# Performance work log

Hardware: AMD Instinct MI355X
Metric: run time of the kernel (lower is better)

The kernel has to match this reference:

```python
import jax, jax.numpy as jnp
import numpy as np

KSIZE = 15
SIGMA = 3.0
PAD = KSIZE // 2


def _gauss_kernel2d():
    g = jnp.arange(KSIZE, dtype=jnp.float32) - KSIZE // 2
    g = jnp.exp(-(g ** 2) / (2.0 * SIGMA * SIGMA))
    g = g / g.sum()
    return g[:, None] * g[None, :]  # [15,15]


def _depthwise_blur(x, k2):
    # x: [B,C,H,W]; 15x15 Gaussian applied per channel (matches per-channel F.conv2d loop)
    C = x.shape[1]
    kernel = jnp.broadcast_to(k2[None, None], (C, 1, KSIZE, KSIZE))
    return jax.lax.conv_general_dilated(
        x, kernel, window_strides=(1, 1), padding=[(PAD, PAD), (PAD, PAD)],
        feature_group_count=C, dimension_numbers=("NCHW", "OIHW", "NCHW"))


def setup_inputs() -> dict:
    key = jax.random.key(0)
    B, C, H, W = 4, 3, 1024, 1024
    x = jax.random.uniform(key, (B, C, H, W), dtype=jnp.float32)
    f32 = lambda v: jnp.asarray(v, dtype=jnp.float32)
    return {
        "x": x,
        "gains": jnp.array([1.1, 1.0, 0.9], dtype=jnp.float32),
        "gamma": f32(0.9),
        "shadow_boost": f32(0.1),
        "highlight_reduce": f32(0.1),
        "brightness": f32(0.05),
        "contrast": f32(1.1),
        "enhance_amount": f32(0.8),
        "softness": f32(0.6),
        "intensity": f32(0.3),
        "rotation": f32(30.0),
        "hardness": f32(2.0),
    }


def reference(x, gains, gamma, shadow_boost, highlight_reduce, brightness,
              contrast, enhance_amount, softness, intensity, rotation, hardness):
    B, C, H, W = x.shape
    k2 = _gauss_kernel2d()

    # WhiteBalanceAdjustment
    x = x * gains.reshape(1, C, 1, 1)
    # ToneCurveAdjustment
    x = jnp.power(x, gamma)
    # ShadowHighlightEnhancement
    hi = jax.nn.sigmoid((x - 0.5) * 10.0)
    x = jnp.clip(x + shadow_boost * (1.0 - hi) - highlight_reduce * hi, 0.0, 1.0)
    # GlobalBrightnessContrastAdjustment
    x = jnp.clip(contrast * (x - 0.5) + 0.5 + brightness, 0.0, 1.0)
    # LocalContrastEnhancement
    local_mean = _depthwise_blur(x, k2)
    x = x + enhance_amount * (x - local_mean)
    # SoftnessFilter
    blurred = _depthwise_blur(x, k2)
    x = softness * blurred + (1.0 - softness) * x
    # GradientNDAdjustment
    ys = jnp.linspace(-1.0, 1.0, H, dtype=jnp.float32)
    xs = jnp.linspace(-1.0, 1.0, W, dtype=jnp.float32)
    grid_y, grid_x = jnp.meshgrid(ys, xs, indexing="ij")
    theta = rotation * (np.pi / 180.0)
    grid_rot = grid_x * jnp.cos(theta) + grid_y * jnp.sin(theta)
    mask = jax.nn.sigmoid(-hardness * grid_rot)[None, None]  # [1,1,H,W]
    x = jnp.clip(x * (1.0 - intensity * mask), 0.0, 1.0)

    return jnp.clip(x, 0.0, 1.0)
```

## Files before the change

### kernel.cpp

```cpp
#include <hip/hip_runtime.h>
#include <math.h>

#define HH 1024
#define WW 1024
#define NPLANES 12
#define PLANE (HH * WW)
#define NTOT (NPLANES * PLANE)

#define TW 64
#define TH 64
#define HR 78
#define PADW 68

struct W15 { float w[15]; };

__global__ __launch_bounds__(256) void k_point(
    const float4* __restrict__ x, float4* __restrict__ o,
    const float* __restrict__ gains,
    const float* __restrict__ pg, const float* __restrict__ psb,
    const float* __restrict__ phr, const float* __restrict__ pbr,
    const float* __restrict__ pct)
{
    int i = blockIdx.x * blockDim.x + threadIdx.x;
    if (i >= NTOT / 4) return;
    int c = ((i * 4) / PLANE) % 3;
    float gain = gains[c];
    float gamma = *pg, sb = *psb, hr = *phr, br = *pbr, ct = *pct;

    float4 v = x[i];
    float* pv = (float*)&v;
#pragma unroll
    for (int j = 0; j < 4; ++j) {
        float t = pv[j] * gain;
        t = __builtin_amdgcn_exp2f(gamma * __log2f(t));
        float hi = __fdividef(1.0f, 1.0f + __expf((0.5f - t) * 10.0f));
        t = t + sb * (1.0f - hi) - hr * hi;
        t = fminf(fmaxf(t, 0.0f), 1.0f);
        t = ct * (t - 0.5f) + 0.5f + br;
        t = fminf(fmaxf(t, 0.0f), 1.0f);
        pv[j] = t;
    }
    o[i] = v;
}

__device__ inline float4 ld4z(const float* __restrict__ row, int x) {
    if (x >= 0 && x + 3 < WW) return *(const float4*)(row + x);
    float4 r; float* p = (float*)&r;
#pragma unroll
    for (int j = 0; j < 4; ++j) { int xx = x + j; p[j] = (xx >= 0 && xx < WW) ? row[xx] : 0.0f; }
    return r;
}

template<int MODE>
__global__ __launch_bounds__(256) void k_blur_fused(
    const float* __restrict__ src, float* __restrict__ dst,
    const float* __restrict__ s0, const float* __restrict__ s1,
    const float* __restrict__ s2, const float* __restrict__ s3, W15 wk)
{
    __shared__ float hbl[HR * PADW];
    const int p   = blockIdx.z;
    const int x0  = blockIdx.x * TW;
    const int y0  = blockIdx.y * TH;
    const int tid = threadIdx.x;
    const float* plane = src + (size_t)p * PLANE;

    {
        const int cx = (tid & 15) * 4;
        const int r0 = tid >> 4;
#pragma unroll
        for (int it = 0; it < 5; ++it) {
            int r = r0 + 16 * it;
            if (r < HR) {
                int y = y0 - 7 + r;
                float4 o;
                if (y >= 0 && y < HH) {
                    const float* row = plane + (size_t)y * WW;
                    int xb = x0 + cx - 8;
                    float f[20];
                    *(float4*)&f[0]  = ld4z(row, xb);
                    *(float4*)&f[4]  = ld4z(row, xb + 4);
                    *(float4*)&f[8]  = ld4z(row, xb + 8);
                    *(float4*)&f[12] = ld4z(row, xb + 12);
                    *(float4*)&f[16] = ld4z(row, xb + 16);
                    float* po = (float*)&o;
#pragma unroll
                    for (int j = 0; j < 4; ++j) {
                        float acc = 0.0f;
#pragma unroll
                        for (int k = 0; k < 15; ++k) acc += wk.w[k] * f[j + 1 + k];
                        po[j] = acc;
                    }
                } else {
                    o = make_float4(0.0f, 0.0f, 0.0f, 0.0f);
                }
                *(float4*)&hbl[r * PADW + cx] = o;
            }
        }
    }
    __syncthreads();

    const int tx  = tid & 63;
    const int ty  = tid >> 6;
    const int ly0 = ty * 16;
    const int x   = x0 + tx;

    float win[15];
#pragma unroll
    for (int k = 0; k < 15; ++k) win[k] = hbl[(ly0 + k) * PADW + tx];

    float a0 = *s0;
    float a1 = 0.f, sth = 0.f, hard = 0.f, base = 0.f;
    if (MODE == 1) {
        a1 = *s1;
        float theta = (*s2) * 0.017453292519943295f;
        float cth = __cosf(theta); sth = __sinf(theta);
        hard = *s3;
        float gx = -1.0f + 2.0f * (float)x * (1.0f / (float)(WW - 1));
        base = gx * cth;
    }

    float* dstP = dst + (size_t)p * PLANE;

#pragma unroll
    for (int j = 0; j < 16; ++j) {
        int y = y0 + ly0 + j;
        float bl = 0.0f;
#pragma unroll
        for (int k = 0; k < 15; ++k) bl += wk.w[k] * win[k];
        float c = plane[(size_t)y * WW + x];
        float v;
        if (MODE == 0) {
            v = (1.0f + a0) * c - a0 * bl;
        } else {
            v = a0 * bl + (1.0f - a0) * c;
            float gy = -1.0f + 2.0f * (float)y * (1.0f / (float)(HH - 1));
            float gr = base + gy * sth;
            float mask = __fdividef(1.0f, 1.0f + __expf(hard * gr));
            v = v * (1.0f - a1 * mask);
            v = fminf(fmaxf(v, 0.0f), 1.0f);
        }
        dstP[(size_t)y * WW + x] = v;
#pragma unroll
        for (int k = 0; k < 14; ++k) win[k] = win[k + 1];
        win[14] = hbl[(ly0 + j + 15) * PADW + tx];
    }
}

extern "C" void kernel_launch(void* const* d_in, const int* in_sizes, int n_in,
                              void* d_out, int out_size, void* d_ws, size_t ws_size,
                              hipStream_t stream)
{
    const float* x       = (const float*)d_in[0];
    const float* gains   = (const float*)d_in[1];
    const float* p_gamma = (const float*)d_in[2];
    const float* p_sb    = (const float*)d_in[3];
    const float* p_hr    = (const float*)d_in[4];
    const float* p_br    = (const float*)d_in[5];
    const float* p_ct    = (const float*)d_in[6];
    const float* p_enh   = (const float*)d_in[7];
    const float* p_soft  = (const float*)d_in[8];
    const float* p_int   = (const float*)d_in[9];
    const float* p_rot   = (const float*)d_in[10];
    const float* p_hard  = (const float*)d_in[11];

    float* A = (float*)d_out;
    float* B = (float*)d_ws;

    W15 wk;
    {
        double g[15], sum = 0.0;
        for (int i = 0; i < 15; ++i) { double d = (double)(i - 7); g[i] = exp(-d * d / 18.0); sum += g[i]; }
        for (int i = 0; i < 15; ++i) wk.w[i] = (float)(g[i] / sum);
    }

    k_point<<<dim3(NTOT / 4 / 256), dim3(256), 0, stream>>>(
        (const float4*)x, (float4*)A, gains, p_gamma, p_sb, p_hr, p_br, p_ct);

    dim3 g(WW / TW, HH / TH, NPLANES);
    k_blur_fused<0><<<g, dim3(256), 0, stream>>>(A, B, p_enh, p_enh, p_enh, p_enh, wk);
    k_blur_fused<1><<<g, dim3(256), 0, stream>>>(B, A, p_soft, p_int, p_rot, p_hard, wk);
}
```

Baseline: 200.3 us.

## Fuse pointwise tone chain into first blur kernel and enlarge final blur tile

The separate pointwise kernel is removed. Each first-blur block now loads its haloed tile of raw input, applies the white-balance/tone/contrast chain while staging it into shared memory, and then blurs from there, which saves one full read and write of the intermediate image. The cost is recomputing the transcendental chain on halo pixels, about 1.6x the pixel count, plus more shared memory per block. The final blur kernel also switches to 128-row tiles with 32 rows per thread, which cuts the vertical halo overhead but halves the block count and raises register pressure.

```diff
diff --git a/kernel.cpp b/kernel.cpp
--- a/kernel.cpp
+++ b/kernel.cpp
@@ -9,73 +9,147 @@
 
 #define TW 64
 #define TH 64
-#define HR 78
-#define PADW 68
+#define HRA 78
+#define RAWP 84
+#define HBLP 68
+
+#define TH2 128
+#define HRB 142
 
 struct W15 { float w[15]; };
 
-__global__ __launch_bounds__(256) void k_point(
-    const float4* __restrict__ x, float4* __restrict__ o,
+__device__ inline float4 ld4z(const float* __restrict__ row, int x) {
+    if (x >= 0 && x + 3 < WW) return *(const float4*)(row + x);
+    float4 r; float* p = (float*)&r;
+#pragma unroll
+    for (int j = 0; j < 4; ++j) { int xx = x + j; p[j] = (xx >= 0 && xx < WW) ? row[xx] : 0.0f; }
+    return r;
+}
+
+__device__ inline float chain1(float t, float gain, float gamma, float sb,
+                               float hr, float br, float ct) {
+    t = t * gain;
+    t = __builtin_amdgcn_exp2f(gamma * __log2f(t));
+    float hi = __fdividef(1.0f, 1.0f + __expf((0.5f - t) * 10.0f));
+    t = t + sb * (1.0f - hi) - hr * hi;
+    t = fminf(fmaxf(t, 0.0f), 1.0f);
+    t = ct * (t - 0.5f) + 0.5f + br;
+    return fminf(fmaxf(t, 0.0f), 1.0f);
+}
+
+__global__ __launch_bounds__(256) void k_chain_blur_lce(
+    const float* __restrict__ x, float* __restrict__ dst,
     const float* __restrict__ gains,
     const float* __restrict__ pg, const float* __restrict__ psb,
     const float* __restrict__ phr, const float* __restrict__ pbr,
-    const float* __restrict__ pct)
+    const float* __restrict__ pct, const float* __restrict__ penh, W15 wk)
 {
-    int i = blockIdx.x * blockDim.x + threadIdx.x;
-    if (i >= NTOT / 4) return;
-    int c = ((i * 4) / PLANE) % 3;
-    float gain = gains[c];
-    float gamma = *pg, sb = *psb, hr = *phr, br = *pbr, ct = *pct;
-
-    float4 v = x[i];
-    float* pv = (float*)&v;
-#pragma unroll
-    for (int j = 0; j < 4; ++j) {
-        float t = pv[j] * gain;
-        t = __builtin_amdgcn_exp2f(gamma * __log2f(t));
-        float hi = __fdividef(1.0f, 1.0f + __expf((0.5f - t) * 10.0f));
-        t = t + sb * (1.0f - hi) - hr * hi;
-        t = fminf(fmaxf(t, 0.0f), 1.0f);
-        t = ct * (t - 0.5f) + 0.5f + br;
-        t = fminf(fmaxf(t, 0.0f), 1.0f);
-        pv[j] = t;
-    }
-    o[i] = v;
-}
-
-__device__ inline float4 ld4z(const float* __restrict__ row, int x) {
-    if (x >= 0 && x + 3 < WW) return *(const float4*)(row + x);
-    float4 r; float* p = (float*)&r;
-#pragma unroll
-    for (int j = 0; j < 4; ++j) { int xx = x + j; p[j] = (xx >= 0 && xx < WW) ? row[xx] : 0.0f; }
-    return r;
-}
-
-template<int MODE>
-__global__ __launch_bounds__(256) void k_blur_fused(
-    const float* __restrict__ src, float* __restrict__ dst,
-    const float* __restrict__ s0, const float* __restrict__ s1,
-    const float* __restrict__ s2, const float* __restrict__ s3, W15 wk)
-{
-    __shared__ float hbl[HR * PADW];
+    __shared__ float raw[HRA * RAWP];
+    __shared__ float hbl[HRA * HBLP];
     const int p   = blockIdx.z;
     const int x0  = blockIdx.x * TW;
     const int y0  = blockIdx.y * TH;
     const int tid = threadIdx.x;
-    const float* plane = src + (size_t)p * PLANE;
+    const float* plane = x + (size_t)p * PLANE;
+
+    const float gain  = gains[p % 3];
+    const float gamma = *pg, sb = *psb, hr = *phr, br = *pbr, ct = *pct;
+    const float e     = *penh;
+
+    for (int i = tid; i < HRA * 20; i += 256) {
+        int r  = i / 20;
+        int c4 = i % 20;
+        int y  = y0 - 7 + r;
+        int xb = x0 - 8 + c4 * 4;
+        float4 v;
+        if (y >= 0 && y < HH) {
+            float4 f = ld4z(plane + (size_t)y * WW, xb);
+            float* pf = (float*)&f; float* pv = (float*)&v;
+#pragma unroll
+            for (int j = 0; j < 4; ++j) {
+                float cv = chain1(pf[j], gain, gamma, sb, hr, br, ct);
+                int xx = xb + j;
+                pv[j] = (xx >= 0 && xx < WW) ? cv : 0.0f;
+            }
+        } else {
+            v = make_float4(0.0f, 0.0f, 0.0f, 0.0f);
+        }
+        *(float4*)&raw[r * RAWP + c4 * 4] = v;
+    }
+    __syncthreads();
 
     {
-        const int cx = (tid & 15) * 4;
+        const int c4 = (tid & 15) * 4;
         const int r0 = tid >> 4;
 #pragma unroll
         for (int it = 0; it < 5; ++it) {
             int r = r0 + 16 * it;
-            if (r < HR) {
+            if (r < HRA) {
+                float f[20];
+#pragma unroll
+                for (int m = 0; m < 5; ++m)
+                    *(float4*)&f[4 * m] = *(const float4*)&raw[r * RAWP + c4 + 4 * m];
+                float4 o; float* po = (float*)&o;
+#pragma unroll
+                for (int j = 0; j < 4; ++j) {
+                    float acc = 0.0f;
+#pragma unroll
+                    for (int k = 0; k < 15; ++k) acc += wk.w[k] * f[j + 1 + k];
+                    po[j] = acc;
+                }
+                *(float4*)&hbl[r * HBLP + c4] = o;
+            }
+        }
+    }
+    __syncthreads();
+
+    const int tx  = tid & 63;
+    const int ty  = tid >> 6;
+    const int ly0 = ty * 16;
+
+    float win[15];
+#pragma unroll
+    for (int k = 0; k < 15; ++k) win[k] = hbl[(ly0 + k) * HBLP + tx];
+
+    float* dstP = dst + (size_t)p * PLANE;
+#pragma unroll
+    for (int j = 0; j < 16; ++j) {
+        int y = y0 + ly0 + j;
+        float lm = 0.0f;
+#pragma unroll
+        for (int k = 0; k < 15; ++k) lm += wk.w[k] * win[k];
+        float c = raw[(ly0 + j + 7) * RAWP + tx + 8];
+        dstP[(size_t)y * WW + x0 + tx] = (1.0f + e) * c - e * lm;
+#pragma unroll
+        for (int k = 0; k < 14; ++k) win[k] = win[k + 1];
+        win[14] = hbl[(ly0 + j + 15) * HBLP + tx];
+    }
+}
+
+__global__ __launch_bounds__(256) void k_blur_final(
+    const float* __restrict__ src, float* __restrict__ dst,
+    const float* __restrict__ psoft, const float* __restrict__ pint,
+    const float* __restrict__ prot, const float* __restrict__ phard, W15 wk)
+{
+    __shared__ float hbl[HRB * HBLP];
+    const int p   = blockIdx.z;
+    const int x0  = blockIdx.x * TW;
+    const int y0  = blockIdx.y * TH2;
+    const int tid = threadIdx.x;
+    const float* plane = src + (size_t)p * PLANE;
+
+    {
+        const int c4 = (tid & 15) * 4;
+        const int r0 = tid >> 4;
+#pragma unroll
+        for (int it = 0; it < 9; ++it) {
+            int r = r0 + 16 * it;
+            if (r < HRB) {
                 int y = y0 - 7 + r;
                 float4 o;
                 if (y >= 0 && y < HH) {
                     const float* row = plane + (size_t)y * WW;
-                    int xb = x0 + cx - 8;
+                    int xb = x0 + c4 - 8;
                     float f[20];
                     *(float4*)&f[0]  = ld4z(row, xb);
                     *(float4*)&f[4]  = ld4z(row, xb + 4);
@@ -93,7 +167,7 @@
                 } else {
                     o = make_float4(0.0f, 0.0f, 0.0f, 0.0f);
                 }
-                *(float4*)&hbl[r * PADW + cx] = o;
+                *(float4*)&hbl[r * HBLP + c4] = o;
             }
         }
     }
@@ -101,48 +175,37 @@
 
     const int tx  = tid & 63;
     const int ty  = tid >> 6;
-    const int ly0 = ty * 16;
+    const int ly0 = ty * 32;
     const int x   = x0 + tx;
 
+    const float s     = *psoft;
+    const float inten = *pint;
+    const float hard  = *phard;
+    const float theta = (*prot) * 0.017453292519943295f;
+    const float cth = __cosf(theta), sth = __sinf(theta);
+    const float base = (-1.0f + 2.0f * (float)x * (1.0f / (float)(WW - 1))) * cth;
+
     float win[15];
 #pragma unroll
-    for (int k = 0; k < 15; ++k) win[k] = hbl[(ly0 + k) * PADW + tx];
-
-    float a0 = *s0;
-    float a1 = 0.f, sth = 0.f, hard = 0.f, base = 0.f;
-    if (MODE == 1) {
-        a1 = *s1;
-        float theta = (*s2) * 0.017453292519943295f;
-        float cth = __cosf(theta); sth = __sinf(theta);
-        hard = *s3;
-        float gx = -1.0f + 2.0f * (float)x * (1.0f / (float)(WW - 1));
-        base = gx * cth;
-    }
+    for (int k = 0; k < 15; ++k) win[k] = hbl[(ly0 + k) * HBLP + tx];
 
     float* dstP = dst + (size_t)p * PLANE;
-
-#pragma unroll
-    for (int j = 0; j < 16; ++j) {
+#pragma unroll
+    for (int j = 0; j < 32; ++j) {
         int y = y0 + ly0 + j;
         float bl = 0.0f;
 #pragma unroll
         for (int k = 0; k < 15; ++k) bl += wk.w[k] * win[k];
         float c = plane[(size_t)y * WW + x];
-        float v;
-        if (MODE == 0) {
-            v = (1.0f + a0) * c - a0 * bl;
-        } else {
-            v = a0 * bl + (1.0f - a0) * c;
-            float gy = -1.0f + 2.0f * (float)y * (1.0f / (float)(HH - 1));
-            float gr = base + gy * sth;
-            float mask = __fdividef(1.0f, 1.0f + __expf(hard * gr));
-            v = v * (1.0f - a1 * mask);
-            v = fminf(fmaxf(v, 0.0f), 1.0f);
-        }
+        float v = s * bl + (1.0f - s) * c;
+        float gy = -1.0f + 2.0f * (float)y * (1.0f / (float)(HH - 1));
+        float mask = __fdividef(1.0f, 1.0f + __expf(hard * (base + gy * sth)));
+        v = v * (1.0f - inten * mask);
+        v = fminf(fmaxf(v, 0.0f), 1.0f);
         dstP[(size_t)y * WW + x] = v;
 #pragma unroll
         for (int k = 0; k < 14; ++k) win[k] = win[k + 1];
-        win[14] = hbl[(ly0 + j + 15) * PADW + tx];
+        win[14] = hbl[(ly0 + j + 15) * HBLP + tx];
     }
 }
 
@@ -163,8 +226,8 @@
     const float* p_rot   = (const float*)d_in[10];
     const float* p_hard  = (const float*)d_in[11];
 
-    float* A = (float*)d_out;
-    float* B = (float*)d_ws;
+    float* X2  = (float*)d_ws;
+    float* OUT = (float*)d_out;
 
     W15 wk;
     {
@@ -173,10 +236,11 @@
         for (int i = 0; i < 15; ++i) wk.w[i] = (float)(g[i] / sum);
     }
 
-    k_point<<<dim3(NTOT / 4 / 256), dim3(256), 0, stream>>>(
-        (const float4*)x, (float4*)A, gains, p_gamma, p_sb, p_hr, p_br, p_ct);
-
-    dim3 g(WW / TW, HH / TH, NPLANES);
-    k_blur_fused<0><<<g, dim3(256), 0, stream>>>(A, B, p_enh, p_enh, p_enh, p_enh, wk);
-    k_blur_fused<1><<<g, dim3(256), 0, stream>>>(B, A, p_soft, p_int, p_rot, p_hard, wk);
-}
+    dim3 ga(WW / TW, HH / TH, NPLANES);
+    k_chain_blur_lce<<<ga, dim3(256), 0, stream>>>(
+        x, X2, gains, p_gamma, p_sb, p_hr, p_br, p_ct, p_enh, wk);
+
+    dim3 gb(WW / TW, HH / TH2, NPLANES);
+    k_blur_final<<<gb, dim3(256), 0, stream>>>(
+        X2, OUT, p_soft, p_int, p_rot, p_hard, wk);
+}
```

Result: no change. 203.0 us (+1.3%).
